# Kernel tuning notes

Hardware: AMD Instinct MI355X
Metric: run time of the kernel (lower is better)

## Reference

```python
import jax, jax.numpy as jnp
import numpy as np
from jax import lax

VOCAB, ENC_DIM, PRED_H, JOINT_H = 4096, 1024, 640, 640
T, MAX_SYM, BLANK, SOS = 128, 30, 0, -1
S = T * (MAX_SYM + 1)  # upper bound on greedy-decode loop iterations


def setup_inputs() -> dict:
    key = jax.random.key(0)
    ks = jax.random.split(key, 10)
    rn = lambda k, shape, s: jax.random.normal(k, shape, jnp.float32) * s
    return {
        "enc_out": rn(ks[0], (1, T, ENC_DIM), 1.0),
        "out_len": T,
        "emb": rn(ks[1], (VOCAB, PRED_H), 0.1),
        "Wih0": rn(ks[2], (4 * PRED_H, PRED_H), 0.04),
        "Whh0": rn(ks[3], (4 * PRED_H, PRED_H), 0.04),
        "b0": jnp.zeros((4 * PRED_H,), jnp.float32),
        "Wih1": rn(ks[4], (4 * PRED_H, PRED_H), 0.04),
        "Whh1": rn(ks[5], (4 * PRED_H, PRED_H), 0.04),
        "b1": jnp.zeros((4 * PRED_H,), jnp.float32),
        "Wj1": rn(ks[6], (JOINT_H, ENC_DIM + PRED_H), 0.03),
        "bj1": jnp.zeros((JOINT_H,), jnp.float32),
        "Wj2": rn(ks[7], (VOCAB, JOINT_H), 0.04),
        "bj2": jnp.zeros((VOCAB,), jnp.float32),
    }


def _lstm_cell(x, h, c, Wih, Whh, b):
    z = x @ Wih.T + h @ Whh.T + b  # [4H], torch gate order i,f,g,o
    i, f, g, o = jnp.split(z, 4)
    c2 = jax.nn.sigmoid(f) * c + jax.nn.sigmoid(i) * jnp.tanh(g)
    return jax.nn.sigmoid(o) * jnp.tanh(c2), c2


def _decode(enc_out, timesteps, emb, Wih0, Whh0, b0, Wih1, Whh1, b1, Wj1, bj1, Wj2, bj2):
    enc = enc_out[0]  # [T, ENC_DIM]

    def step(carry, _):
        t, sa, last, h0, c0, h1, c1, labels, cnt, done = carry
        # prediction net step (SOS = -1 -> zero embedding)
        g_in = jnp.where(last < 0, 0.0, emb[jnp.maximum(last, 0)])
        h0n, c0n = _lstm_cell(g_in, h0, c0, Wih0, Whh0, b0)
        h1n, c1n = _lstm_cell(h0n, h1, c1, Wih1, Whh1, b1)
        # joint net on current encoder frame
        f = enc[jnp.minimum(t, T - 1)]
        hid = jax.nn.relu(Wj1 @ jnp.concatenate([f, h1n]) + bj1)
        logits = Wj2 @ hid + bj2  # [VOCAB]
        k = jnp.argmax(logits).astype(jnp.int32)
        stop_sym = (k == BLANK) | (sa >= MAX_SYM)
        emit = (~stop_sym) & (~done)
        adv = stop_sym & (~done)
        # emit: append symbol, keep hidden'; blank/max: advance time, discard hidden'
        last2 = jnp.where(emit, k, last)
        h0 = jnp.where(emit, h0n, h0); c0 = jnp.where(emit, c0n, c0)
        h1 = jnp.where(emit, h1n, h1); c1 = jnp.where(emit, c1n, c1)
        labels = labels.at[cnt].set(jnp.where(emit, k, labels[cnt]))
        cnt2 = cnt + emit.astype(jnp.int32)
        sa2 = jnp.where(emit, sa + 1, jnp.where(adv, 0, sa))
        t2 = t + adv.astype(jnp.int32)
        done2 = done | (adv & (t2 >= timesteps))
        out_logits = jnp.where(done, 0.0, logits)
        return (t2, sa2, last2, h0, c0, h1, c1, labels, cnt2, done2), out_logits

    zeros = jnp.zeros((PRED_H,), jnp.float32)
    carry0 = (jnp.int32(0), jnp.int32(0), jnp.int32(SOS),
              zeros, zeros, zeros, zeros,
              jnp.full((S,), -1, jnp.int32), jnp.int32(0), jnp.bool_(False))
    carry, logits_seq = lax.scan(step, carry0, None, length=S)
    labels, cnt = carry[7], carry[8]
    return logits_seq, labels, cnt


def reference(enc_out, out_len, emb, Wih0, Whh0, b0, Wih1, Whh1, b1, Wj1, bj1, Wj2, bj2):
    return _decode(enc_out, out_len, emb, Wih0, Whh0, b0, Wih1, Whh1, b1, Wj1, bj1, Wj2, bj2)
```

## Files before the change

### kernel.cpp

```cpp
#include <hip/hip_runtime.h>
#include <cmath>

#define VOCAB   4096
#define ENC_DIM 1024
#define PRED_H  640
#define JOINT_H 640
#define TMAX    128
#define MAX_SYM 30
#define NSTEPS  (TMAX*(MAX_SYM+1))
#define NWG     160
#define NTHR    512
#define RLX __ATOMIC_RELAXED
#define AGT __HIP_MEMORY_SCOPE_AGENT

typedef unsigned long long u64;
typedef __attribute__((ext_vector_type(4))) float f32x4;
typedef __attribute__((ext_vector_type(4))) unsigned int u32x4;


__device__ __forceinline__ float wave_red(float v){
  v += __shfl_xor(v, 32, 64);
  v += __shfl_xor(v, 16, 64);
  v += __shfl_xor(v,  8, 64);
  v += __shfl_xor(v,  4, 64);
  v += __shfl_xor(v,  2, 64);
  v += __shfl_xor(v,  1, 64);
  return v;
}

__device__ __forceinline__ float sigf(float x){ return 1.0f/(1.0f+expf(-x)); }

__device__ __forceinline__ void sendline(u64* base, int w, f32x4 hv, unsigned tag){
  u32x4 a, b;
  a.x = __float_as_uint(hv.x); a.y = tag; a.z = __float_as_uint(hv.y); a.w = tag;
  b.x = __float_as_uint(hv.z); b.y = tag; b.z = __float_as_uint(hv.w); b.w = tag;
  u64* p = base + ((size_t)w<<3);
  asm volatile("global_store_dwordx4 %0, %2, off sc0 sc1\n\t"
               "global_store_dwordx4 %1, %3, off sc0 sc1"
               :: "v"(p), "v"(p+2), "v"(a), "v"(b) : "memory");
}

__device__ __forceinline__ void pollline(const u64* base, float* dstLDS,
                                         unsigned tag, int i){
  const u64* p = base + ((size_t)i<<3);
  u32x4 v0, v1;
  for(;;){
    asm volatile("global_load_dwordx4 %0, %2, off sc0 sc1\n\t"
                 "global_load_dwordx4 %1, %3, off sc0 sc1\n\t"
                 "s_waitcnt vmcnt(0)"
                 : "=&v"(v0), "=&v"(v1) : "v"(p), "v"(p+2) : "memory");
    if (v0.y == tag && v0.w == tag && v1.y == tag && v1.w == tag) break;
    __builtin_amdgcn_s_sleep(1);
  }
  __builtin_amdgcn_sched_barrier(0);
  float* d = dstLDS + (i<<2);
  d[0] = __uint_as_float(v0.x);
  d[1] = __uint_as_float(v0.z);
  d[2] = __uint_as_float(v1.x);
  d[3] = __uint_as_float(v1.z);
}

__device__ __forceinline__ u64 mkentry(float lg, int r, unsigned ep){
  unsigned u = __float_as_uint(lg);
  u = (u & 0x80000000u) ? ~u : (u | 0x80000000u);
  return ((u64)u<<24) | ((u64)(ep&0xFFFu)<<12) | (u64)(4095 - r);
}

__global__ void init_ws(unsigned* ws){
  for (int i = threadIdx.x; i < 10240; i += 256) ws[i] = 0u;
}

__global__ __launch_bounds__(NTHR, 2)
void rnnt_decode(const float* __restrict__ enc,
                 const int*   __restrict__ outlen_p,
                 const float* __restrict__ emb,
                 const float* __restrict__ Wih0, const float* __restrict__ Whh0, const float* __restrict__ b0,
                 const float* __restrict__ Wih1, const float* __restrict__ Whh1, const float* __restrict__ b1,
                 const float* __restrict__ Wj1,  const float* __restrict__ bj1,
                 const float* __restrict__ Wj2,  const float* __restrict__ bj2,
                 float* __restrict__ out,
                 char* __restrict__ ws)
{
  const int wg = blockIdx.x, tid = threadIdx.x;
  const int wave = tid >> 6, lane = tid & 63;
  const int timesteps = outlen_p[0];

  u64* dataA = (u64*)(ws);
  u64* dataB = (u64*)(ws + 10240);
  u64* dataH = (u64*)(ws + 20480);
  u64* parts = (u64*)(ws + 30720);

  __shared__ float xa[PRED_H];
  __shared__ float xsh[ENC_DIM];
  __shared__ float h0buf[2][PRED_H];
  __shared__ float h1buf[2][PRED_H];
  __shared__ float hidsh[JOINT_H];
  __shared__ float zsh[4][4];
  __shared__ float zjsA[8], zjsB[8];
  __shared__ float c0c[4], c1c[4], c0p[4], c1p[4];
  __shared__ float bj1sh[4];
  __shared__ u64 psh[8];
  __shared__ u64 pmx[3];

  const int jb = wg*4;

  const int gA = wave & 3;
  const int jA = wave >> 2;
  const int rowA = gA*PRED_H + jb + jA;
  const int rowB = gA*PRED_H + jb + jA + 2;

  float w0xA[10], w0hA[10], w0xB[10], w0hB[10];
  float w1xA[10], w1hA[10], w1xB[10], w1hB[10];
  #pragma unroll
  for (int i = 0; i < 10; ++i){
    int c = lane + (i<<6);
    w0xA[i] = Wih0[(size_t)rowA*PRED_H + c];
    w0hA[i] = Whh0[(size_t)rowA*PRED_H + c];
    w1xA[i] = Wih1[(size_t)rowA*PRED_H + c];
    w1hA[i] = Whh1[(size_t)rowA*PRED_H + c];
    w0xB[i] = Wih0[(size_t)rowB*PRED_H + c];
    w0hB[i] = Whh0[(size_t)rowB*PRED_H + c];
    w1xB[i] = Wih1[(size_t)rowB*PRED_H + c];
    w1hB[i] = Whh1[(size_t)rowB*PRED_H + c];
  }
  const float bA0 = b0[rowA], bA1 = b1[rowA];
  const float bB0 = b0[rowB], bB1 = b1[rowB];

  const int grp = wave >> 2;
  const int vt  = ((wave & 3)<<6) | lane;
  const int rP0 = jb + grp;
  const int rP1 = jb + 2 + grp;
  float wjf0[4], wjh0[3], wjf1[4], wjh1[3];
  #pragma unroll
  for (int i = 0; i < 4; ++i){
    wjf0[i] = Wj1[(size_t)rP0*(ENC_DIM+PRED_H) + vt + (i<<8)];
    wjf1[i] = Wj1[(size_t)rP1*(ENC_DIM+PRED_H) + vt + (i<<8)];
  }
  #pragma unroll
  for (int i = 0; i < 3; ++i){
    int c = vt + (i<<8);
    wjh0[i] = (c < PRED_H) ? Wj1[(size_t)rP0*(ENC_DIM+PRED_H) + ENC_DIM + c] : 0.f;
    wjh1[i] = (c < PRED_H) ? Wj1[(size_t)rP1*(ENC_DIM+PRED_H) + ENC_DIM + c] : 0.f;
  }
  float ca0 = 0.f, ca1 = 0.f;

  const int nrows = (wg < 96) ? 26 : 25;
  const int r2b = wg*25 + (wg < 96 ? wg : 96);
  float wj2[4][10], bj2r[4];
  #pragma unroll
  for (int p = 0; p < 4; ++p){
    bool act = (p*8 + wave) < nrows;
    int r = act ? (r2b + p*8 + wave) : 0;
    #pragma unroll
    for (int i = 0; i < 10; ++i)
      wj2[p][i] = act ? Wj2[(size_t)r*JOINT_H + lane + (i<<6)] : 0.f;
    bj2r[p] = act ? bj2[r] : 0.f;
  }

  for (int i = tid; i < PRED_H; i += NTHR){ h0buf[0][i] = 0.f; h1buf[0][i] = 0.f; }
  if (tid < 4){ c0c[tid] = 0.f; c1c[tid] = 0.f; bj1sh[tid] = bj1[jb+tid]; }
  __syncthreads();

  int cur = 0, t = 0, sa = 0, last = -1, cnt = 0, tStaged = -1;
  bool done = false, reuse = false;

  for (int s = 0; s < NSTEPS; ++s){
    if (done){
      if (wg < 8) out[(size_t)s*VOCAB + wg*NTHR + tid] = 0.f;
      continue;
    }
    const unsigned tag = (unsigned)(s + 1);

    if (!reuse){
      for (int i = tid; i < PRED_H; i += NTHR)
        xa[i] = (last >= 0) ? emb[(size_t)last*PRED_H + i] : 0.f;
      __syncthreads();
      {
        float acc = 0.f;
        #pragma unroll
        for (int i = 0; i < 10; ++i) acc = fmaf(w0xA[i], xa[lane+(i<<6)], acc);
        #pragma unroll
        for (int i = 0; i < 10; ++i) acc = fmaf(w0hA[i], h0buf[cur][lane+(i<<6)], acc);
        acc = wave_red(acc);
        if (lane == 0) zsh[gA][jA] = acc + bA0;
        float a2 = 0.f;
        #pragma unroll
        for (int i = 0; i < 10; ++i) a2 = fmaf(w0xB[i], xa[lane+(i<<6)], a2);
        #pragma unroll
        for (int i = 0; i < 10; ++i) a2 = fmaf(w0hB[i], h0buf[cur][lane+(i<<6)], a2);
        a2 = wave_red(a2);
        if (lane == 0) zsh[gA][jA+2] = a2 + bB0;
      }
      __syncthreads();
      if (wave == 0){
        float hv = 0.f;
        if (lane < 4){
          float ig = sigf(zsh[0][lane]), fg = sigf(zsh[1][lane]);
          float gg = tanhf(zsh[2][lane]), og = sigf(zsh[3][lane]);
          float c2 = fg*c0c[lane] + ig*gg;
          c0p[lane] = c2;
          hv = og*tanhf(c2);
        }
        f32x4 v;
        v.x = __shfl(hv, 0, 64); v.y = __shfl(hv, 1, 64);
        v.z = __shfl(hv, 2, 64); v.w = __shfl(hv, 3, 64);
        if (lane == 0) sendline(dataA, wg, v, tag);
      }

      if (tid < 160) pollline(dataA, h0buf[cur^1], tag, tid);
      __syncthreads();
      {
        float acc = 0.f;
        #pragma unroll
        for (int i = 0; i < 10; ++i) acc = fmaf(w1xA[i], h0buf[cur^1][lane+(i<<6)], acc);
        #pragma unroll
        for (int i = 0; i < 10; ++i) acc = fmaf(w1hA[i], h1buf[cur][lane+(i<<6)], acc);
        acc = wave_red(acc);
        if (lane == 0) zsh[gA][jA] = acc + bA1;
        float a2 = 0.f;
        #pragma unroll
        for (int i = 0; i < 10; ++i) a2 = fmaf(w1xB[i], h0buf[cur^1][lane+(i<<6)], a2);
        #pragma unroll
        for (int i = 0; i < 10; ++i) a2 = fmaf(w1hB[i], h1buf[cur][lane+(i<<6)], a2);
        a2 = wave_red(a2);
        if (lane == 0) zsh[gA][jA+2] = a2 + bB1;
      }
      __syncthreads();
      if (wave == 0){
        float hv = 0.f;
        if (lane < 4){
          float ig = sigf(zsh[0][lane]), fg = sigf(zsh[1][lane]);
          float gg = tanhf(zsh[2][lane]), og = sigf(zsh[3][lane]);
          float c2 = fg*c1c[lane] + ig*gg;
          c1p[lane] = c2;
          hv = og*tanhf(c2);
        }
        f32x4 v;
        v.x = __shfl(hv, 0, 64); v.y = __shfl(hv, 1, 64);
        v.z = __shfl(hv, 2, 64); v.w = __shfl(hv, 3, 64);
        if (lane == 0) sendline(dataB, wg, v, tag);
      }
    }

    {
      int tcap = (t < TMAX-1) ? t : (TMAX-1);
      bool fNew = (tcap != tStaged);
      if (fNew)
        for (int i = tid; i < ENC_DIM; i += NTHR) xsh[i] = enc[(size_t)tcap*ENC_DIM + i];
      if (!reuse){
        if (tid < 160) pollline(dataB, h1buf[cur^1], tag, tid);
      }
      __syncthreads();
      if (fNew){
        float a = 0.f, b = 0.f;
        #pragma unroll
        for (int i = 0; i < 4; ++i){
          a = fmaf(wjf0[i], xsh[vt+(i<<8)], a);
          b = fmaf(wjf1[i], xsh[vt+(i<<8)], b);
        }
        ca0 = a; ca1 = b;
        tStaged = tcap;
      }
      {
        float acc = ca0;
        #pragma unroll
        for (int i = 0; i < 3; ++i){
          int c = vt + (i<<8);
          acc = fmaf(wjh0[i], h1buf[cur^1][(c < PRED_H) ? c : 0], acc);
        }
        acc = wave_red(acc);
        if (lane == 0) zjsA[wave] = acc;
        float acc2 = ca1;
        #pragma unroll
        for (int i = 0; i < 3; ++i){
          int c = vt + (i<<8);
          acc2 = fmaf(wjh1[i], h1buf[cur^1][(c < PRED_H) ? c : 0], acc2);
        }
        acc2 = wave_red(acc2);
        if (lane == 0) zjsB[wave] = acc2;
      }
      __syncthreads();
      if (wave == 0){
        float hv = 0.f;
        if (lane < 4){
          float v;
          if (lane == 0)      v = zjsA[0]+zjsA[1]+zjsA[2]+zjsA[3] + bj1sh[0];
          else if (lane == 1) v = zjsA[4]+zjsA[5]+zjsA[6]+zjsA[7] + bj1sh[1];
          else if (lane == 2) v = zjsB[0]+zjsB[1]+zjsB[2]+zjsB[3] + bj1sh[2];
          else                v = zjsB[4]+zjsB[5]+zjsB[6]+zjsB[7] + bj1sh[3];
          hv = v > 0.f ? v : 0.f;
        }
        f32x4 v;
        v.x = __shfl(hv, 0, 64); v.y = __shfl(hv, 1, 64);
        v.z = __shfl(hv, 2, 64); v.w = __shfl(hv, 3, 64);
        if (lane == 0) sendline(dataH, wg, v, tag);
      }
    }

    int k;
    {
      if (tid < 160) pollline(dataH, hidsh, tag, tid);
      __syncthreads();
      u64 best = 0;
      #pragma unroll
      for (int p = 0; p < 4; ++p){
        if (p*8 + wave < nrows){
          int r = r2b + p*8 + wave;
          float acc = 0.f;
          #pragma unroll
          for (int i = 0; i < 10; ++i) acc = fmaf(wj2[p][i], hidsh[lane+(i<<6)], acc);
          acc = wave_red(acc);
          if (lane == 0){
            float lg = acc + bj2r[p];
            out[(size_t)s*VOCAB + r] = lg;
            u64 e = mkentry(lg, r, tag);
            if (e > best) best = e;
          }
        }
      }
      if (lane == 0) psh[wave] = best;
      __syncthreads();
      if (tid == 0){
        u64 m = psh[0];
        #pragma unroll
        for (int w = 1; w < 8; ++w) if (psh[w] > m) m = psh[w];
        __hip_atomic_store(&parts[(size_t)wg<<3], m, RLX, AGT);
      }
      u64 myp = 0;
      if (tid < 160){
        for(;;){
          u64 e = __hip_atomic_load(&parts[(size_t)tid<<3], RLX, AGT);
          if ((unsigned)((e>>12) & 0xFFFu) == (tag & 0xFFFu)){ myp = e; break; }
          __builtin_amdgcn_s_sleep(1);
        }
      }
      if (wave < 3){
        #pragma unroll
        for (int off = 32; off; off >>= 1){
          u64 o = __shfl_xor(myp, off, 64);
          if (o > myp) myp = o;
        }
        if (lane == 0) pmx[wave] = myp;
      }
      __syncthreads();
      u64 m = pmx[0];
      if (pmx[1] > m) m = pmx[1];
      if (pmx[2] > m) m = pmx[2];
      k = 4095 - (int)(m & 0xFFFull);
    }

    bool stop = (k == 0) || (sa >= MAX_SYM);
    if (!stop){
      if (wg == 0 && tid == 0) out[(size_t)NSTEPS*VOCAB + cnt] = (float)k;
      if (tid < 4){ c0c[tid] = c0p[tid]; c1c[tid] = c1p[tid]; }
      cnt++; sa++; last = k; cur ^= 1; reuse = false;
    } else {
      sa = 0; t++; reuse = true;
      if (t >= timesteps) done = true;
    }
    __syncthreads();
  }

  size_t lab = (size_t)NSTEPS*VOCAB;
  int gidx = wg*NTHR + tid;
  for (int i = cnt + gidx; i < NSTEPS; i += NWG*NTHR) out[lab + i] = -1.f;
  if (wg == 0 && tid == 0) out[lab + NSTEPS] = (float)cnt;
}

extern "C" void kernel_launch(void* const* d_in, const int* in_sizes, int n_in,
                              void* d_out, int out_size, void* d_ws, size_t ws_size,
                              hipStream_t stream) {
  const float* enc  = (const float*)d_in[0];
  const int*   olen = (const int*)  d_in[1];
  const float* emb  = (const float*)d_in[2];
  const float* Wih0 = (const float*)d_in[3];
  const float* Whh0 = (const float*)d_in[4];
  const float* b0   = (const float*)d_in[5];
  const float* Wih1 = (const float*)d_in[6];
  const float* Whh1 = (const float*)d_in[7];
  const float* b1   = (const float*)d_in[8];
  const float* Wj1  = (const float*)d_in[9];
  const float* bj1  = (const float*)d_in[10];
  const float* Wj2  = (const float*)d_in[11];
  const float* bj2  = (const float*)d_in[12];
  float* out = (float*)d_out;
  char* ws = (char*)d_ws;

  init_ws<<<1, 256, 0, stream>>>((unsigned*)d_ws);

  void* args[] = {&enc,&olen,&emb,&Wih0,&Whh0,&b0,&Wih1,&Whh1,&b1,
                  &Wj1,&bj1,&Wj2,&bj2,&out,&ws};
  hipLaunchCooperativeKernel((const void*)rnnt_decode, dim3(NWG), dim3(NTHR),
                             args, 0, stream);
}
```

Baseline: 50.17 ms.

## Precompute recurrent matvecs during argmax wait and load embeddings into registers

The h·Whh parts of both LSTM layers are now computed speculatively from the candidate new hidden states while each workgroup waits for the cross-workgroup argmax partials. This takes half of each LSTM matvec off the serial step chain. The embedding row is read straight into registers, which removes the shared staging buffer and one barrier. Launch bounds drop to one block per CU so more registers are available. The speculative sums are only valid when the candidate state is the one actually committed, so the handling of blank/advance steps has to match exactly.

```diff
diff --git a/kernel.cpp b/kernel.cpp
--- a/kernel.cpp
+++ b/kernel.cpp
@@ -70,7 +70,7 @@
   for (int i = threadIdx.x; i < 10240; i += 256) ws[i] = 0u;
 }
 
-__global__ __launch_bounds__(NTHR, 2)
+__global__ __launch_bounds__(NTHR, 1)
 void rnnt_decode(const float* __restrict__ enc,
                  const int*   __restrict__ outlen_p,
                  const float* __restrict__ emb,
@@ -90,7 +90,6 @@
   u64* dataH = (u64*)(ws + 20480);
   u64* parts = (u64*)(ws + 30720);
 
-  __shared__ float xa[PRED_H];
   __shared__ float xsh[ENC_DIM];
   __shared__ float h0buf[2][PRED_H];
   __shared__ float h1buf[2][PRED_H];
@@ -157,12 +156,14 @@
     bj2r[p] = act ? bj2[r] : 0.f;
   }
 
-  for (int i = tid; i < PRED_H; i += NTHR){ h0buf[0][i] = 0.f; h1buf[0][i] = 0.f; }
+  for (int i = tid; i < PRED_H; i += NTHR){ h0buf[0][i] = 0.f; h1buf[0][i] = 0.f;
+                                            h0buf[1][i] = 0.f; h1buf[1][i] = 0.f; }
   if (tid < 4){ c0c[tid] = 0.f; c1c[tid] = 0.f; bj1sh[tid] = bj1[jb+tid]; }
   __syncthreads();
 
   int cur = 0, t = 0, sa = 0, last = -1, cnt = 0, tStaged = -1;
   bool done = false, reuse = false;
+  float s0A = 0.f, s0B = 0.f, s1A = 0.f, s1B = 0.f;
 
   for (int s = 0; s < NSTEPS; ++s){
     if (done){
@@ -172,24 +173,25 @@
     const unsigned tag = (unsigned)(s + 1);
 
     if (!reuse){
-      for (int i = tid; i < PRED_H; i += NTHR)
-        xa[i] = (last >= 0) ? emb[(size_t)last*PRED_H + i] : 0.f;
-      __syncthreads();
       {
-        float acc = 0.f;
-        #pragma unroll
-        for (int i = 0; i < 10; ++i) acc = fmaf(w0xA[i], xa[lane+(i<<6)], acc);
-        #pragma unroll
-        for (int i = 0; i < 10; ++i) acc = fmaf(w0hA[i], h0buf[cur][lane+(i<<6)], acc);
-        acc = wave_red(acc);
-        if (lane == 0) zsh[gA][jA] = acc + bA0;
-        float a2 = 0.f;
-        #pragma unroll
-        for (int i = 0; i < 10; ++i) a2 = fmaf(w0xB[i], xa[lane+(i<<6)], a2);
-        #pragma unroll
-        for (int i = 0; i < 10; ++i) a2 = fmaf(w0hB[i], h0buf[cur][lane+(i<<6)], a2);
-        a2 = wave_red(a2);
-        if (lane == 0) zsh[gA][jA+2] = a2 + bB0;
+        float XA = 0.f, XB = 0.f;
+        if (last >= 0){
+          float xr[10];
+          #pragma unroll
+          for (int i = 0; i < 10; ++i)
+            xr[i] = emb[(size_t)last*PRED_H + lane + (i<<6)];
+          #pragma unroll
+          for (int i = 0; i < 10; ++i){
+            XA = fmaf(w0xA[i], xr[i], XA);
+            XB = fmaf(w0xB[i], xr[i], XB);
+          }
+          XA = wave_red(XA);
+          XB = wave_red(XB);
+        }
+        if (lane == 0){
+          zsh[gA][jA]   = XA + s0A + bA0;
+          zsh[gA][jA+2] = XB + s0B + bB0;
+        }
       }
       __syncthreads();
       if (wave == 0){
@@ -210,20 +212,19 @@
       if (tid < 160) pollline(dataA, h0buf[cur^1], tag, tid);
       __syncthreads();
       {
-        float acc = 0.f;
-        #pragma unroll
-        for (int i = 0; i < 10; ++i) acc = fmaf(w1xA[i], h0buf[cur^1][lane+(i<<6)], acc);
-        #pragma unroll
-        for (int i = 0; i < 10; ++i) acc = fmaf(w1hA[i], h1buf[cur][lane+(i<<6)], acc);
-        acc = wave_red(acc);
-        if (lane == 0) zsh[gA][jA] = acc + bA1;
-        float a2 = 0.f;
-        #pragma unroll
-        for (int i = 0; i < 10; ++i) a2 = fmaf(w1xB[i], h0buf[cur^1][lane+(i<<6)], a2);
-        #pragma unroll
-        for (int i = 0; i < 10; ++i) a2 = fmaf(w1hB[i], h1buf[cur][lane+(i<<6)], a2);
-        a2 = wave_red(a2);
-        if (lane == 0) zsh[gA][jA+2] = a2 + bB1;
+        float XA = 0.f, XB = 0.f;
+        #pragma unroll
+        for (int i = 0; i < 10; ++i){
+          float h0 = h0buf[cur^1][lane+(i<<6)];
+          XA = fmaf(w1xA[i], h0, XA);
+          XB = fmaf(w1xB[i], h0, XB);
+        }
+        XA = wave_red(XA);
+        XB = wave_red(XB);
+        if (lane == 0){
+          zsh[gA][jA]   = XA + s1A + bA1;
+          zsh[gA][jA+2] = XB + s1B + bB1;
+        }
       }
       __syncthreads();
       if (wave == 0){
@@ -326,6 +327,22 @@
         for (int w = 1; w < 8; ++w) if (psh[w] > m) m = psh[w];
         __hip_atomic_store(&parts[(size_t)wg<<3], m, RLX, AGT);
       }
+
+      {
+        float a0 = 0.f, b0v = 0.f, a1 = 0.f, b1v = 0.f;
+        #pragma unroll
+        for (int i = 0; i < 10; ++i){
+          float h0p = h0buf[cur^1][lane+(i<<6)];
+          float h1p = h1buf[cur^1][lane+(i<<6)];
+          a0  = fmaf(w0hA[i], h0p, a0);
+          b0v = fmaf(w0hB[i], h0p, b0v);
+          a1  = fmaf(w1hA[i], h1p, a1);
+          b1v = fmaf(w1hB[i], h1p, b1v);
+        }
+        s0A = wave_red(a0);  s0B = wave_red(b0v);
+        s1A = wave_red(a1);  s1B = wave_red(b1v);
+      }
+
       u64 myp = 0;
       if (tid < 160){
         for(;;){
```

Result: faster. 41.60 ms (-17.1%).
